# Optimization experiments

Hardware: AMD Instinct MI355X
Metric: run time of the kernel (lower is better)

The kernel has to match this reference:

```python
import jax, jax.numpy as jnp
import numpy as np

NY, NX = 1024, 2048
DX, DT, NU, UB = 1.0, 0.1, 0.01, 1.0
NITER = 5
NLEVEL = int(np.log2(NY)) + 1  # 11
DIAG = -8.0 / (3.0 * DX * DX)  # center coefficient of the Laplacian stencil wA


def _conv(x, w, stride=1):
    # single-channel 'VALID' cross-correlation, same semantics as torch Conv2d(padding=0)
    return jax.lax.conv_general_dilated(x, w, (stride, stride), 'VALID',
                                        dimension_numbers=('NCHW', 'OIHW', 'NCHW'))


def _bc_u(u):
    # inlet (left/top/bottom) = ub, zero-gradient outflow on the right
    uu = jnp.pad(u, ((0, 0), (0, 0), (1, 1), (1, 1)))
    uu = uu.at[:, :, :, 0].set(UB)
    uu = uu.at[:, :, :, -1].set(uu[:, :, :, -2])
    uu = uu.at[:, :, 0, :].set(UB)
    uu = uu.at[:, :, -1, :].set(UB)
    return uu


def _bc_v(v):
    # v = 0 on inlet/top/bottom (zero pad), zero-gradient outflow on the right
    vv = jnp.pad(v, ((0, 0), (0, 0), (1, 1), (1, 1)))
    vv = vv.at[:, :, :, -1].set(vv[:, :, :, -2])
    return vv


def _bc_p(p):
    # zero-gradient pressure except fixed p=0 at the outlet
    pp = jnp.pad(p, ((0, 0), (0, 0), (1, 1), (1, 1)))
    pp = pp.at[:, :, :, 0].set(pp[:, :, :, 1])
    pp = pp.at[:, :, :, -1].set(0.0)
    pp = pp.at[:, :, 0, :].set(pp[:, :, 1, :])
    pp = pp.at[:, :, -1, :].set(pp[:, :, -2, :])
    return pp


def _bc_cw(a):
    # homogeneous (zero) halo for the multigrid correction
    return jnp.pad(a, ((0, 0), (0, 0), (1, 1), (1, 1)))


def _prolong(a):
    return jnp.repeat(jnp.repeat(a, 2, axis=2), 2, axis=3)


def _f_cycle_mg(uu, vv, p, w_xadv, w_yadv, w_A, w_res):
    b = -(_conv(uu, w_xadv) + _conv(vv, w_yadv)) / DT
    for _ in range(NITER):
        r = _conv(_bc_p(p), w_A) - b
        r_s = [r]
        for _i in range(1, NLEVEL):
            r = _conv(r, w_res, stride=2)
            r_s.append(r)
        a = jnp.zeros((1, 1, 1, 1), dtype=p.dtype)
        for i in reversed(range(1, NLEVEL)):
            if i == NLEVEL - 1:
                a = r_s[i] / DIAG
            else:
                a = a - _conv(_bc_cw(a), w_A) / DIAG + r_s[i] / DIAG
            a = _prolong(a)
        p = p - a
        p = p - _conv(_bc_p(p), w_A) / DIAG + b / DIAG
    return p


def _forward(u, v, p, sigma, w_xadv, w_yadv, w_diff, w_A, w_res):
    uu, vv, pp = _bc_u(u), _bc_v(v), _bc_p(p)
    Grapx_p = _conv(pp, w_xadv) * DT
    Grapy_p = _conv(pp, w_yadv) * DT
    ADx_u, ADy_u = _conv(uu, w_xadv), _conv(uu, w_yadv)
    ADx_v, ADy_v = _conv(vv, w_xadv), _conv(vv, w_yadv)
    AD2_u, AD2_v = _conv(uu, w_diff), _conv(vv, w_diff)
    # predictor half-step
    bu = u + 0.5 * (NU * AD2_u * DT - u * ADx_u * DT - v * ADy_u * DT) - Grapx_p
    bv = v + 0.5 * (NU * AD2_v * DT - u * ADx_v * DT - v * ADy_v * DT) - Grapy_p
    damp = 1.0 / (1.0 + DT * sigma)  # solid body Brinkman penalty
    bu, bv = bu * damp, bv * damp
    buu, bvv = _bc_u(bu), _bc_v(bv)
    ADx_u, ADy_u = _conv(buu, w_xadv), _conv(buu, w_yadv)
    ADx_v, ADy_v = _conv(bvv, w_xadv), _conv(bvv, w_yadv)
    AD2_u, AD2_v = _conv(buu, w_diff), _conv(bvv, w_diff)
    # corrector step
    u = u + NU * AD2_u * DT - bu * ADx_u * DT - bv * ADy_u * DT - Grapx_p
    v = v + NU * AD2_v * DT - bu * ADx_v * DT - bv * ADy_v * DT - Grapy_p
    u, v = u * damp, v * damp
    uu, vv = _bc_u(u), _bc_v(v)
    # pressure solve via multigrid F-cycle + projection
    p = _f_cycle_mg(uu, vv, p, w_xadv, w_yadv, w_A, w_res)
    pp = _bc_p(p)
    u = u - _conv(pp, w_xadv) * DT
    v = v - _conv(pp, w_yadv) * DT
    u, v = u * damp, v * damp
    return jnp.concatenate([u, v, p], axis=1)  # (1, 3, NY, NX)


def setup_inputs() -> dict:
    key = jax.random.key(0)
    k1, k2, k3 = jax.random.split(key, 3)
    shp = (1, 1, NY, NX)
    u = jax.random.normal(k1, shp, jnp.float32) * 0.1 + UB
    v = jax.random.normal(k2, shp, jnp.float32) * 0.1
    p = jax.random.normal(k3, shp, jnp.float32) * 0.1
    # bluff-body mask: 1/timescale inside the rectangle (Block.create_solid_body_2D)
    cor_x, cor_y = NX // 4, NY // 2
    size_x, size_y = NX // 32, NY // 8
    sigma = jnp.zeros(shp, jnp.float32)
    sigma = sigma.at[0, 0, cor_y - size_y:cor_y + size_y,
                     cor_x - size_x:cor_x + size_x].set(1e8)
    # finite-difference stencils from get_weights_linear_2D(dx)
    w_diff = jnp.array([[1., 1., 1.], [1., -8., 1.], [1., 1., 1.]],
                       jnp.float32).reshape(1, 1, 3, 3) / (3.0 * DX * DX)
    w_xadv = jnp.array([[-1., 0., 1.], [-4., 0., 4.], [-1., 0., 1.]],
                       jnp.float32).reshape(1, 1, 3, 3) / (12.0 * DX)
    w_yadv = jnp.array([[-1., -4., -1.], [0., 0., 0.], [1., 4., 1.]],
                       jnp.float32).reshape(1, 1, 3, 3) / (12.0 * DX)
    w_A = w_diff
    w_res = jnp.full((1, 1, 2, 2), 0.25, jnp.float32)
    return {"u": u, "v": v, "p": p, "sigma": sigma, "w_xadv": w_xadv,
            "w_yadv": w_yadv, "w_diff": w_diff, "w_A": w_A, "w_res": w_res}


def reference(u, v, p, sigma, w_xadv, w_yadv, w_diff, w_A, w_res):
    return _forward(u, v, p, sigma, w_xadv, w_yadv, w_diff, w_A, w_res)
```

## Files before the change

kernel.cpp:

```cpp
#include <hip/hip_runtime.h>
#include <cstdint>

#define GNY 1024
#define GNX 2048
#define GNPTS (GNY * GNX)

namespace {
constexpr float DT = 0.1f;
constexpr float NUc = 0.01f;
constexpr float INV_DIAG = -0.375f;
}

__device__ __forceinline__ float bc_u_at(const float* __restrict__ f, int y, int x) {
    if (y < 0 || y >= GNY || x < 0) return 1.0f;
    if (x >= GNX) x = GNX - 1;
    return f[y * GNX + x];
}
__device__ __forceinline__ float bc_v_at(const float* __restrict__ f, int y, int x) {
    if (y < 0 || y >= GNY || x < 0) return 0.0f;
    if (x >= GNX) x = GNX - 1;
    return f[y * GNX + x];
}
__device__ __forceinline__ float bc_p_at(const float* __restrict__ f, int y, int x) {
    if (x >= GNX) return 0.0f;
    if (x < 0) x = 0;
    y = min(max(y, 0), GNY - 1);
    return f[y * GNX + x];
}

__device__ __forceinline__ float conv_x3(const float m[3][3]) {
    return ((m[0][2] - m[0][0]) + 4.0f * (m[1][2] - m[1][0]) + (m[2][2] - m[2][0])) * (1.0f / 12.0f);
}
__device__ __forceinline__ float conv_y3(const float m[3][3]) {
    return ((m[2][0] - m[0][0]) + 4.0f * (m[2][1] - m[0][1]) + (m[2][2] - m[0][2])) * (1.0f / 12.0f);
}
__device__ __forceinline__ float conv_d3(const float m[3][3]) {
    return (m[0][0] + m[0][1] + m[0][2] + m[1][0] + m[1][2] + m[2][0] + m[2][1] + m[2][2]
            - 8.0f * m[1][1]) * (1.0f / 3.0f);
}

__device__ __forceinline__ float strip_d3(const float* b0, const float* b1, const float* b2, int k) {
    float cs0 = b0[k] + b1[k] + b2[k];
    float cs1 = b0[k+1] + b1[k+1] + b2[k+1];
    float cs2 = b0[k+2] + b1[k+2] + b2[k+2];
    return (cs0 + cs1 + cs2 - 9.0f * b1[k+1]) * (1.0f / 3.0f);
}
__device__ __forceinline__ float strip_x3(const float* b0, const float* b1, const float* b2, int k) {
    return ((b0[k+2] + 4.0f*b1[k+2] + b2[k+2]) - (b0[k] + 4.0f*b1[k] + b2[k])) * (1.0f / 12.0f);
}
__device__ __forceinline__ float strip_y3(const float* b0, const float* b1, const float* b2, int k) {
    return ((b2[k] - b0[k]) + 4.0f*(b2[k+1] - b0[k+1]) + (b2[k+2] - b0[k+2])) * (1.0f / 12.0f);
}
#define STRIP_LOAD(arr, base, stride) \
    { _Pragma("unroll") for (int j = 0; j < 6; ++j) { \
        b0[j] = arr[(base) + j]; b1[j] = arr[(base) + (stride) + j]; b2[j] = arr[(base) + 2*(stride) + j]; } }

__global__ __launch_bounds__(256) void k_front(
        const float* __restrict__ u, const float* __restrict__ v,
        const float* __restrict__ p, const float* __restrict__ sigma,
        float* __restrict__ u2g, float* __restrict__ v2g, float* __restrict__ bg,
        float* __restrict__ r1, float* __restrict__ r2, float* __restrict__ r3,
        float* __restrict__ r4, float* __restrict__ r5) {
    __shared__ float scrF[7110];
    float* sP    = scrF;
    float* sU    = scrF + 1482;
    float* sV    = scrF + 2964;
    float* sU2   = scrF + 1482;
    float* sV2   = scrF + 2672;
    float* sBu   = scrF + 4446;
    float* sBv   = scrF + 5778;
    float* s0    = scrF + 4446;
    float* s1    = scrF + 5502;
    float* s2    = scrF + 5774;
    float* s3    = scrF + 5846;
    float* s4    = scrF + 5866;

    int t = threadIdx.x;
    int bx = blockIdx.x, by = blockIdx.y;
    int y0 = by * 32, x0 = bx * 32;
    bool edge = !(bx >= 1 && bx <= 62 && by >= 1 && by <= 30);
    bool rightcol = (bx == 63);

    if (!edge) {
        for (int i = t; i < 1444; i += 256) {
            int wy = i / 38, wx = i - wy * 38;
            int idx = (y0 - 3 + wy) * GNX + (x0 - 3 + wx);
            sP[wy * 39 + wx] = p[idx];
            sU[wy * 39 + wx] = u[idx];
            sV[wy * 39 + wx] = v[idx];
        }
    } else {
        for (int i = t; i < 1444; i += 256) {
            int wy = i / 38, wx = i - wy * 38;
            int gy = y0 - 3 + wy, gx = x0 - 3 + wx;
            sP[wy * 39 + wx] = bc_p_at(p, gy, gx);
            sU[wy * 39 + wx] = bc_u_at(u, gy, gx);
            sV[wy * 39 + wx] = bc_v_at(v, gy, gx);
        }
    }
    __syncthreads();

    if (!edge) {
        for (int s = t; s < 324; s += 256) {
            int ay = s / 9, ax0 = (s - (s / 9) * 9) * 4;
            int base = ay * 39 + ax0;
            float b0[6], b1[6], b2[6];
            float d3u[4], x3u[4], y3u[4], uc4[4];
            STRIP_LOAD(sU, base, 39)
#pragma unroll
            for (int k = 0; k < 4; ++k) {
                uc4[k] = b1[k+1];
                d3u[k] = strip_d3(b0, b1, b2, k);
                x3u[k] = strip_x3(b0, b1, b2, k);
                y3u[k] = strip_y3(b0, b1, b2, k);
            }
            float d3v[4], x3v[4], y3v[4], vc4[4];
            STRIP_LOAD(sV, base, 39)
#pragma unroll
            for (int k = 0; k < 4; ++k) {
                vc4[k] = b1[k+1];
                d3v[k] = strip_d3(b0, b1, b2, k);
                x3v[k] = strip_x3(b0, b1, b2, k);
                y3v[k] = strip_y3(b0, b1, b2, k);
            }
            float gx4[4], gy4[4];
            STRIP_LOAD(sP, base, 39)
#pragma unroll
            for (int k = 0; k < 4; ++k) {
                gx4[k] = strip_x3(b0, b1, b2, k) * DT;
                gy4[k] = strip_y3(b0, b1, b2, k) * DT;
            }
#pragma unroll
            for (int k = 0; k < 4; ++k) {
                int gy = y0 - 2 + ay, gx = x0 - 2 + ax0 + k;
                float dampv = 1.0f / (1.0f + DT * sigma[gy * GNX + gx]);
                float buv = (uc4[k] + 0.5f * (NUc * d3u[k] * DT - uc4[k] * x3u[k] * DT - vc4[k] * y3u[k] * DT) - gx4[k]) * dampv;
                float bvv = (vc4[k] + 0.5f * (NUc * d3v[k] * DT - uc4[k] * x3v[k] * DT - vc4[k] * y3v[k] * DT) - gy4[k]) * dampv;
                sBu[ay * 37 + ax0 + k] = buv;
                sBv[ay * 37 + ax0 + k] = bvv;
            }
        }
    } else {
        for (int i = t; i < 1296; i += 256) {
            int ay = i / 36, ax = i - ay * 36;
            int gy = y0 - 2 + ay, gx = x0 - 2 + ax;
            float un[3][3], vn[3][3], pn[3][3];
#pragma unroll
            for (int dy = 0; dy < 3; ++dy)
#pragma unroll
                for (int dx = 0; dx < 3; ++dx) {
                    int li = (ay + dy) * 39 + ax + dx;
                    un[dy][dx] = sU[li]; vn[dy][dx] = sV[li]; pn[dy][dx] = sP[li];
                }
            float buv, bvv;
            bool valid = (gy >= 0 && gy < GNY && gx >= 0 && gx < GNX);
            if (valid) {
                float dampv = 1.0f / (1.0f + DT * sigma[gy * GNX + gx]);
                float gxp = conv_x3(pn) * DT, gyp = conv_y3(pn) * DT;
                float uc = un[1][1], vc = vn[1][1];
                buv = (uc + 0.5f * (NUc * conv_d3(un) * DT - uc * conv_x3(un) * DT - vc * conv_y3(un) * DT) - gxp) * dampv;
                bvv = (vc + 0.5f * (NUc * conv_d3(vn) * DT - uc * conv_x3(vn) * DT - vc * conv_y3(vn) * DT) - gyp) * dampv;
            } else if (gy < 0 || gy >= GNY || gx < 0) {
                buv = 1.0f; bvv = 0.0f;
            } else {
                buv = 0.0f; bvv = 0.0f;
            }
            sBu[ay * 37 + ax] = buv;
            sBv[ay * 37 + ax] = bvv;
        }
    }
    __syncthreads();

    float ucS[2][4], vcS[2][4];
    float ucA[5], vcA[5];
    if (!edge) {
        int ns = 0;
        for (int s = t; s < 306; s += 256, ++ns) {
            int cy = s / 9, cx0 = (s - (s / 9) * 9) * 4;
#pragma unroll
            for (int k = 0; k < 4; ++k) {
                if (cx0 + k < 34) {
                    int li = (cy + 2) * 39 + cx0 + 2 + k;
                    ucS[ns][k] = sU[li]; vcS[ns][k] = sV[li];
                }
            }
        }
    } else {
        int np = 0;
        for (int i = t; i < 1156; i += 256, ++np) {
            int cy = i / 34, cx = i - cy * 34;
            int li = (cy + 2) * 39 + cx + 2;
            ucA[np] = sU[li]; vcA[np] = sV[li];
        }
    }
    __syncthreads();
    if (!edge) {
        int ns = 0;
        for (int s = t; s < 306; s += 256, ++ns) {
            int cy = s / 9, cx0 = (s - (s / 9) * 9) * 4;
            int baseB = cy * 37 + cx0;
            int baseP = (cy + 1) * 39 + cx0 + 1;
            float b0[6], b1[6], b2[6];
            float d3bu[4], x3bu[4], y3bu[4], buc4[4];
            STRIP_LOAD(sBu, baseB, 37)
#pragma unroll
            for (int k = 0; k < 4; ++k) {
                buc4[k] = b1[k+1];
                d3bu[k] = strip_d3(b0, b1, b2, k);
                x3bu[k] = strip_x3(b0, b1, b2, k);
                y3bu[k] = strip_y3(b0, b1, b2, k);
            }
            float d3bv[4], x3bv[4], y3bv[4], bvc4[4];
            STRIP_LOAD(sBv, baseB, 37)
#pragma unroll
            for (int k = 0; k < 4; ++k) {
                bvc4[k] = b1[k+1];
                d3bv[k] = strip_d3(b0, b1, b2, k);
                x3bv[k] = strip_x3(b0, b1, b2, k);
                y3bv[k] = strip_y3(b0, b1, b2, k);
            }
            float gx4[4], gy4[4];
            STRIP_LOAD(sP, baseP, 39)
#pragma unroll
            for (int k = 0; k < 4; ++k) {
                gx4[k] = strip_x3(b0, b1, b2, k) * DT;
                gy4[k] = strip_y3(b0, b1, b2, k) * DT;
            }
#pragma unroll
            for (int k = 0; k < 4; ++k) {
                if (cx0 + k < 34) {
                    int cy_ = cy, cx_ = cx0 + k;
                    int gyy = y0 - 1 + cy_, gxx = x0 - 1 + cx_;
                    int idx = gyy * GNX + gxx;
                    float dampv = 1.0f / (1.0f + DT * sigma[idx]);
                    float u2_ = (ucS[ns][k] + NUc * d3bu[k] * DT - buc4[k] * x3bu[k] * DT - bvc4[k] * y3bu[k] * DT - gx4[k]) * dampv;
                    float v2_ = (vcS[ns][k] + NUc * d3bv[k] * DT - buc4[k] * x3bv[k] * DT - bvc4[k] * y3bv[k] * DT - gy4[k]) * dampv;
                    if (cy_ >= 1 && cy_ <= 32 && cx_ >= 1 && cx_ <= 32) {
                        u2g[idx] = u2_; v2g[idx] = v2_;
                    }
                    sU2[cy_ * 35 + cx_] = u2_;
                    sV2[cy_ * 35 + cx_] = v2_;
                }
            }
        }
    } else {
        int np = 0;
        for (int i = t; i < 1156; i += 256, ++np) {
            int cy = i / 34, cx = i - cy * 34;
            int gy = y0 - 1 + cy, gx = x0 - 1 + cx;
            float u2_ = 0.0f, v2_ = 0.0f;
            bool valid = (gy >= 0 && gy < GNY && gx >= 0 && gx < GNX);
            if (valid) {
                float bun[3][3], bvn[3][3], pn[3][3];
                if (!rightcol) {
#pragma unroll
                    for (int dy = 0; dy < 3; ++dy)
#pragma unroll
                        for (int dx = 0; dx < 3; ++dx) {
                            int li = (cy + dy) * 37 + cx + dx;
                            bun[dy][dx] = sBu[li]; bvn[dy][dx] = sBv[li];
                            pn[dy][dx] = sP[(cy + dy + 1) * 39 + cx + dx + 1];
                        }
                } else {
#pragma unroll
                    for (int dy = 0; dy < 3; ++dy)
#pragma unroll
                        for (int dx = 0; dx < 3; ++dx) {
                            int yy = gy + dy - 1, xx = gx + dx - 1;
                            pn[dy][dx] = sP[(cy + dy + 1) * 39 + cx + dx + 1];
                            if (yy < 0 || yy >= GNY || xx < 0) { bun[dy][dx] = 1.0f; bvn[dy][dx] = 0.0f; }
                            else {
                                int cxx = (xx >= GNX) ? GNX - 1 : xx;
                                int li = (cy + dy) * 37 + (cxx - (x0 - 2));
                                bun[dy][dx] = sBu[li]; bvn[dy][dx] = sBv[li];
                            }
                        }
                }
                int idx = gy * GNX + gx;
                float gxp = conv_x3(pn) * DT, gyp = conv_y3(pn) * DT;
                float dampv = 1.0f / (1.0f + DT * sigma[idx]);
                float buc = bun[1][1], bvc = bvn[1][1];
                u2_ = (ucA[np] + NUc * conv_d3(bun) * DT - buc * conv_x3(bun) * DT - bvc * conv_y3(bun) * DT - gxp) * dampv;
                v2_ = (vcA[np] + NUc * conv_d3(bvn) * DT - buc * conv_x3(bvn) * DT - bvc * conv_y3(bvn) * DT - gyp) * dampv;
                if (cy >= 1 && cy <= 32 && cx >= 1 && cx <= 32) {
                    u2g[idx] = u2_; v2g[idx] = v2_;
                }
            } else if (gy < 0 || gy >= GNY || gx < 0) {
                u2_ = 1.0f; v2_ = 0.0f;
            }
            sU2[cy * 35 + cx] = u2_;
            sV2[cy * 35 + cx] = v2_;
        }
    }
    __syncthreads();

    if (!rightcol) {
        int ty = t >> 3, tx0 = (t & 7) * 4;
        int baseU = ty * 35 + tx0;
        int baseP = (ty + 2) * 39 + tx0 + 2;
        float b0[6], b1[6], b2[6];
        float x3u[4];
        STRIP_LOAD(sU2, baseU, 35)
#pragma unroll
        for (int k = 0; k < 4; ++k) x3u[k] = strip_x3(b0, b1, b2, k);
        float y3v[4];
        STRIP_LOAD(sV2, baseU, 35)
#pragma unroll
        for (int k = 0; k < 4; ++k) y3v[k] = strip_y3(b0, b1, b2, k);
        float d3p[4];
        STRIP_LOAD(sP, baseP, 39)
#pragma unroll
        for (int k = 0; k < 4; ++k) d3p[k] = strip_d3(b0, b1, b2, k);
#pragma unroll
        for (int k = 0; k < 4; ++k) {
            float b_ = -(x3u[k] + y3v[k]) * (1.0f / DT);
            bg[(y0 + ty) * GNX + x0 + tx0 + k] = b_;
            s0[ty * 33 + tx0 + k] = d3p[k] - b_;
        }
    } else {
        for (int i = t; i < 1024; i += 256) {
            int ty = i >> 5, tx = i & 31;
            int gy = y0 + ty, gx = x0 + tx;
            float un[3][3], vn[3][3], pn[3][3];
#pragma unroll
            for (int dy = 0; dy < 3; ++dy)
#pragma unroll
                for (int dx = 0; dx < 3; ++dx) {
                    int yy = gy + dy - 1, xx = gx + dx - 1;
                    pn[dy][dx] = sP[(ty + dy + 2) * 39 + tx + dx + 2];
                    if (yy < 0 || yy >= GNY || xx < 0) { un[dy][dx] = 1.0f; vn[dy][dx] = 0.0f; }
                    else {
                        int cxx = (xx >= GNX) ? GNX - 1 : xx;
                        int li = (ty + dy) * 35 + (cxx - (x0 - 1));
                        un[dy][dx] = sU2[li]; vn[dy][dx] = sV2[li];
                    }
                }
            float b_ = -(conv_x3(un) + conv_y3(vn)) * (1.0f / DT);
            bg[gy * GNX + gx] = b_;
            s0[ty * 33 + tx] = conv_d3(pn) - b_;
        }
    }
    __syncthreads();

    { int qy = t >> 4, qx = t & 15;
      float vv = 0.25f * (s0[(2*qy)*33 + 2*qx] + s0[(2*qy)*33 + 2*qx + 1]
                        + s0[(2*qy+1)*33 + 2*qx] + s0[(2*qy+1)*33 + 2*qx + 1]);
      s1[qy*17 + qx] = vv;
      r1[(by*16 + qy)*1024 + bx*16 + qx] = vv; }
    __syncthreads();
    if (t < 64) { int qy = t >> 3, qx = t & 7;
      float vv = 0.25f * (s1[(2*qy)*17 + 2*qx] + s1[(2*qy)*17 + 2*qx + 1]
                        + s1[(2*qy+1)*17 + 2*qx] + s1[(2*qy+1)*17 + 2*qx + 1]);
      s2[qy*9 + qx] = vv;
      r2[(by*8 + qy)*512 + bx*8 + qx] = vv; }
    __syncthreads();
    if (t < 16) { int qy = t >> 2, qx = t & 3;
      float vv = 0.25f * (s2[(2*qy)*9 + 2*qx] + s2[(2*qy)*9 + 2*qx + 1]
                        + s2[(2*qy+1)*9 + 2*qx] + s2[(2*qy+1)*9 + 2*qx + 1]);
      s3[qy*5 + qx] = vv;
      r3[(by*4 + qy)*256 + bx*4 + qx] = vv; }
    __syncthreads();
    if (t < 4) { int qy = t >> 1, qx = t & 1;
      float vv = 0.25f * (s3[(2*qy)*5 + 2*qx] + s3[(2*qy)*5 + 2*qx + 1]
                        + s3[(2*qy+1)*5 + 2*qx] + s3[(2*qy+1)*5 + 2*qx + 1]);
      s4[qy*3 + qx] = vv;
      r4[(by*2 + qy)*128 + bx*2 + qx] = vv; }
    __syncthreads();
    if (t == 0)
        r5[by*64 + bx] = 0.25f * (s4[0] + s4[1] + s4[3] + s4[4]);
}

__global__ __launch_bounds__(256) void k_mg(
        const float* __restrict__ p_src, const float* __restrict__ b,
        const float* __restrict__ r1, const float* __restrict__ r2,
        const float* __restrict__ r3, const float* __restrict__ r4,
        const float* __restrict__ r5,
        float* __restrict__ p_dst,
        float* __restrict__ o1, float* __restrict__ o2, float* __restrict__ o3,
        float* __restrict__ o4, float* __restrict__ o5,
        const float* __restrict__ sigma, float* __restrict__ u_io,
        float* __restrict__ v_io, int last) {
    __shared__ float scr[3948];
    __shared__ float w6v[9], w5v[9], w4v[16], w3v[36], w2v[100], w1v[324];
    float* s5  = scr;
    float* s6  = scr + 2048;
    float* s7  = scr + 2560;
    float* s8  = scr + 2688;
    float* s9  = scr + 2720;
    float* s10 = scr + 2728;
    float* a9  = scr + 2730;
    float* a8  = scr + 2738;
    float* a7  = scr + 2770;
    float* sPp = scr;
    float* sPn = scr + 1332;
    float* s0  = scr + 2522;
    float* s1  = scr + 3578;
    float* s2  = scr + 3850;
    float* s3  = scr + 3922;
    float* s4  = scr + 3942;

    int t = threadIdx.x;
    int bx = blockIdx.x, by = blockIdx.y;
    int y0 = by * 32, x0 = bx * 32;
    bool interior = (bx >= 1 && bx <= 62 && by >= 1 && by <= 30);

    for (int i = t; i < 2048; i += 256) s5[i] = r5[i];
    __syncthreads();
    for (int i = t; i < 512; i += 256) {
        int y = i >> 5, x = i & 31;
        s6[i] = 0.25f * (s5[(2*y)*64 + 2*x] + s5[(2*y)*64 + 2*x + 1]
                       + s5[(2*y+1)*64 + 2*x] + s5[(2*y+1)*64 + 2*x + 1]);
    }
    __syncthreads();
    if (t < 128) { int y = t >> 4, x = t & 15;
        s7[t] = 0.25f * (s6[(2*y)*32 + 2*x] + s6[(2*y)*32 + 2*x + 1]
                       + s6[(2*y+1)*32 + 2*x] + s6[(2*y+1)*32 + 2*x + 1]); }
    __syncthreads();
    if (t < 32) { int y = t >> 3, x = t & 7;
        s8[t] = 0.25f * (s7[(2*y)*16 + 2*x] + s7[(2*y)*16 + 2*x + 1]
                       + s7[(2*y+1)*16 + 2*x] + s7[(2*y+1)*16 + 2*x + 1]); }
    __syncthreads();
    if (t < 8) { int y = t >> 2, x = t & 3;
        s9[t] = 0.25f * (s8[(2*y)*8 + 2*x] + s8[(2*y)*8 + 2*x + 1]
                       + s8[(2*y+1)*8 + 2*x] + s8[(2*y+1)*8 + 2*x + 1]); }
    __syncthreads();
    if (t < 2)
        s10[t] = 0.25f * (s9[2*t] + s9[2*t + 1] + s9[4 + 2*t] + s9[4 + 2*t + 1]);
    __syncthreads();

    auto upv = [&](auto pget, float rval, int H, int W, int y, int x) -> float {
        float m[3][3];
#pragma unroll
        for (int dy = 0; dy < 3; ++dy)
#pragma unroll
            for (int dx = 0; dx < 3; ++dx) {
                int yy = y + dy - 1, xx = x + dx - 1;
                m[dy][dx] = (yy >= 0 && yy < H && xx >= 0 && xx < W) ? pget(yy >> 1, xx >> 1) : 0.0f;
            }
        float conv = (m[0][0] + m[0][1] + m[0][2] + m[1][0] + m[1][2]
                      + m[2][0] + m[2][1] + m[2][2] - 8.0f * m[1][1]) * (1.0f / 3.0f);
        return m[1][1] - conv * INV_DIAG + rval * INV_DIAG;
    };

    if (t < 8) { int y = t >> 2, x = t & 3;
        a9[t] = upv([&](int py, int px) { return s10[py*2 + px] * INV_DIAG; },
                    s9[t], 2, 4, y, x); }
    __syncthreads();
    if (t < 32) { int y = t >> 3, x = t & 7;
        a8[t] = upv([&](int py, int px) { return a9[py*4 + px]; },
                    s8[t], 4, 8, y, x); }
    __syncthreads();
    if (t < 128) { int y = t >> 4, x = t & 15;
        a7[t] = upv([&](int py, int px) { return a8[py*8 + px]; },
                    s7[t], 8, 16, y, x); }
    __syncthreads();

    int w6ylo = (by - 2) >> 1, w6xlo = (bx - 2) >> 1;
    int w5ylo = by - 1,        w5xlo = bx - 1;
    int w4ylo = 2*by - 1,      w4xlo = 2*bx - 1;
    int w3ylo = 4*by - 1,      w3xlo = 4*bx - 1;
    int w2ylo = 8*by - 1,      w2xlo = 8*bx - 1;
    int w1ylo = 16*by - 1,     w1xlo = 16*bx - 1;

    if (t < 9) { int gy = w6ylo + t/3, gx = w6xlo + t%3;
        w6v[t] = (gy >= 0 && gy < 16 && gx >= 0 && gx < 32)
            ? upv([&](int py, int px) { return a7[py*16 + px]; },
                  s6[gy*32 + gx], 16, 32, gy, gx) : 0.0f; }
    __syncthreads();
    if (t < 9) { int gy = w5ylo + t/3, gx = w5xlo + t%3;
        w5v[t] = (gy >= 0 && gy < 32 && gx >= 0 && gx < 64)
            ? upv([&](int py, int px) { return w6v[(py - w6ylo)*3 + (px - w6xlo)]; },
                  s5[gy*64 + gx], 32, 64, gy, gx) : 0.0f; }
    __syncthreads();
    if (t < 16) { int gy = w4ylo + t/4, gx = w4xlo + t%4;
        w4v[t] = (gy >= 0 && gy < 64 && gx >= 0 && gx < 128)
            ? upv([&](int py, int px) { return w5v[(py - w5ylo)*3 + (px - w5xlo)]; },
                  r4[gy*128 + gx], 64, 128, gy, gx) : 0.0f; }
    __syncthreads();
    if (t < 36) { int gy = w3ylo + t/6, gx = w3xlo + t%6;
        w3v[t] = (gy >= 0 && gy < 128 && gx >= 0 && gx < 256)
            ? upv([&](int py, int px) { return w4v[(py - w4ylo)*4 + (px - w4xlo)]; },
                  r3[gy*256 + gx], 128, 256, gy, gx) : 0.0f; }
    __syncthreads();
    if (t < 100) { int gy = w2ylo + t/10, gx = w2xlo + t%10;
        w2v[t] = (gy >= 0 && gy < 256 && gx >= 0 && gx < 512)
            ? upv([&](int py, int px) { return w3v[(py - w3ylo)*6 + (px - w3xlo)]; },
                  r2[gy*512 + gx], 256, 512, gy, gx) : 0.0f; }
    __syncthreads();
    for (int i = t; i < 324; i += 256) { int gy = w1ylo + i/18, gx = w1xlo + i%18;
        w1v[i] = (gy >= 0 && gy < 512 && gx >= 0 && gx < 1024)
            ? upv([&](int py, int px) { return w2v[(py - w2ylo)*10 + (px - w2xlo)]; },
                  r1[gy*1024 + gx], 512, 1024, gy, gx) : 0.0f; }
    __syncthreads();

    for (int i = t; i < 1296; i += 256) {
        int wy = i / 36, wx = i - wy * 36;
        int yy = y0 - 2 + wy, xx = x0 - 2 + wx;
        float v = 0.0f;
        if (xx < GNX) {
            int cy = min(max(yy, 0), GNY - 1);
            int cx = xx < 0 ? 0 : xx;
            v = p_src[cy*GNX + cx] - w1v[((cy >> 1) - w1ylo)*18 + ((cx >> 1) - w1xlo)];
        }
        sPp[wy*37 + wx] = v;
    }
    __syncthreads();
    if (interior) {
        for (int s = t; s < 306; s += 256) {
            int wy = s / 9, wx0 = (s - (s / 9) * 9) * 4;
            int base = wy * 37 + wx0;
            float b0[6], b1[6], b2[6];
            STRIP_LOAD(sPp, base, 37)
#pragma unroll
            for (int k = 0; k < 4; ++k) {
                if (wx0 + k < 34) {
                    float c = b1[k+1];
                    float conv = strip_d3(b0, b1, b2, k);
                    float bvv = b[(y0 - 1 + wy) * GNX + (x0 - 1 + wx0 + k)];
                    sPn[wy * 35 + wx0 + k] = c - conv * INV_DIAG + bvv * INV_DIAG;
                }
            }
        }
    } else {
        for (int i = t; i < 1156; i += 256) {
            int wy = i / 34, wx = i - wy * 34;
            int yy = y0 - 1 + wy, xx = x0 - 1 + wx;
            float v = 0.0f;
            if (xx < GNX) {
                int cy = min(max(yy, 0), GNY - 1);
                int cx = xx < 0 ? 0 : xx;
                int rb = cy - y0 + 2, cb = cx - x0 + 2;
                float m[3][3];
#pragma unroll
                for (int dy = 0; dy < 3; ++dy)
#pragma unroll
                    for (int dx = 0; dx < 3; ++dx)
                        m[dy][dx] = sPp[(rb + dy - 1)*37 + (cb + dx - 1)];
                float conv = (m[0][0] + m[0][1] + m[0][2] + m[1][0] + m[1][2]
                              + m[2][0] + m[2][1] + m[2][2] - 8.0f*m[1][1]) * (1.0f / 3.0f);
                v = m[1][1] - conv * INV_DIAG + b[cy*GNX + cx] * INV_DIAG;
            }
            sPn[wy*35 + wx] = v;
        }
    }
    __syncthreads();
    for (int i = t; i < 1024; i += 256) {
        int ty = i >> 5, tx = i & 31;
        p_dst[(y0 + ty)*GNX + x0 + tx] = sPn[(ty + 1)*35 + (tx + 1)];
    }

    if (!last) {
        {
            int ty = t >> 3, tx0 = (t & 7) * 4;
            int base = ty * 35 + tx0;
            float b0[6], b1[6], b2[6];
            STRIP_LOAD(sPn, base, 35)
#pragma unroll
            for (int k = 0; k < 4; ++k) {
                float d3 = strip_d3(b0, b1, b2, k);
                s0[ty * 33 + tx0 + k] = d3 - b[(y0 + ty) * GNX + x0 + tx0 + k];
            }
        }
        __syncthreads();
        { int qy = t >> 4, qx = t & 15;
          float v = 0.25f * (s0[(2*qy)*33 + 2*qx] + s0[(2*qy)*33 + 2*qx + 1]
                           + s0[(2*qy+1)*33 + 2*qx] + s0[(2*qy+1)*33 + 2*qx + 1]);
          s1[qy*17 + qx] = v;
          o1[(by*16 + qy)*1024 + bx*16 + qx] = v; }
        __syncthreads();
        if (t < 64) { int qy = t >> 3, qx = t & 7;
          float v = 0.25f * (s1[(2*qy)*17 + 2*qx] + s1[(2*qy)*17 + 2*qx + 1]
                           + s1[(2*qy+1)*17 + 2*qx] + s1[(2*qy+1)*17 + 2*qx + 1]);
          s2[qy*9 + qx] = v;
          o2[(by*8 + qy)*512 + bx*8 + qx] = v; }
        __syncthreads();
        if (t < 16) { int qy = t >> 2, qx = t & 3;
          float v = 0.25f * (s2[(2*qy)*9 + 2*qx] + s2[(2*qy)*9 + 2*qx + 1]
                           + s2[(2*qy+1)*9 + 2*qx] + s2[(2*qy+1)*9 + 2*qx + 1]);
          s3[qy*5 + qx] = v;
          o3[(by*4 + qy)*256 + bx*4 + qx] = v; }
        __syncthreads();
        if (t < 4) { int qy = t >> 1, qx = t & 1;
          float v = 0.25f * (s3[(2*qy)*5 + 2*qx] + s3[(2*qy)*5 + 2*qx + 1]
                           + s3[(2*qy+1)*5 + 2*qx] + s3[(2*qy+1)*5 + 2*qx + 1]);
          s4[qy*3 + qx] = v;
          o4[(by*2 + qy)*128 + bx*2 + qx] = v; }
        __syncthreads();
        if (t == 0)
            o5[by*64 + bx] = 0.25f * (s4[0] + s4[1] + s4[3] + s4[4]);
    } else {
        int ty = t >> 3, tx0 = (t & 7) * 4;
        int base = ty * 35 + tx0;
        float b0[6], b1[6], b2[6];
        float x3p[4], y3p[4];
        STRIP_LOAD(sPn, base, 35)
#pragma unroll
        for (int k = 0; k < 4; ++k) {
            x3p[k] = strip_x3(b0, b1, b2, k);
            y3p[k] = strip_y3(b0, b1, b2, k);
        }
#pragma unroll
        for (int k = 0; k < 4; ++k) {
            int idx = (y0 + ty) * GNX + x0 + tx0 + k;
            float damp = 1.0f / (1.0f + DT * sigma[idx]);
            u_io[idx] = (u_io[idx] - x3p[k] * DT) * damp;
            v_io[idx] = (v_io[idx] - y3p[k] * DT) * damp;
        }
    }
}

extern "C" void kernel_launch(void* const* d_in, const int* in_sizes, int n_in,
                              void* d_out, int out_size, void* d_ws, size_t ws_size,
                              hipStream_t stream) {
    (void)in_sizes; (void)n_in; (void)out_size; (void)ws_size;
    const float* u_in  = (const float*)d_in[0];
    const float* v_in  = (const float*)d_in[1];
    const float* p_in  = (const float*)d_in[2];
    const float* sigma = (const float*)d_in[3];

    float* out_u = (float*)d_out;
    float* out_v = out_u + GNPTS;
    float* out_p = out_u + 2 * (size_t)GNPTS;

    float* ws   = (float*)d_ws;
    float* b    = ws;
    float* p_ws = b + (size_t)GNPTS;
    float* base = p_ws + (size_t)GNPTS;
    float* A_[5], * B_[5];
    size_t lsz[5] = {524288, 131072, 32768, 8192, 2048};
    float* cur = base;
    for (int l = 0; l < 5; ++l) { A_[l] = cur; cur += lsz[l]; }
    for (int l = 0; l < 5; ++l) { B_[l] = cur; cur += lsz[l]; }

    dim3 grdT(GNX / 32, GNY / 32), blkT(256);

    k_front<<<grdT, blkT, 0, stream>>>(u_in, v_in, p_in, sigma,
                                       out_u, out_v, b,
                                       A_[0], A_[1], A_[2], A_[3], A_[4]);

    const float* p_cur = p_in;
    float* p_bufs[2] = { out_p, p_ws };
    for (int it = 0; it < 5; ++it) {
        float** rp = (it % 2 == 0) ? A_ : B_;
        float** wp = (it % 2 == 0) ? B_ : A_;
        float* p_next = p_bufs[it % 2];
        int last = (it == 4) ? 1 : 0;
        k_mg<<<grdT, blkT, 0, stream>>>(p_cur, b,
                                        rp[0], rp[1], rp[2], rp[3], rp[4],
                                        p_next,
                                        wp[0], wp[1], wp[2], wp[3], wp[4],
                                        sigma, out_u, out_v, last);
        p_cur = p_next;
    }
}
```

Baseline: 219.9 us.

## Use 6-wide stencil strips and swizzle block indices for locality

Interior stencil passes now give each thread 6 output columns instead of 4. This removes the second loop trip for threads past 256, so each pass fits in one wave of work with fewer redundant shared-memory halo reads per output. Block IDs are remapped with a swizzle so that consecutively scheduled blocks cover nearby tiles, which is meant to improve L2 locality for halo reuse. Shared arrays are padded slightly to absorb the wider strip reads. The cost is higher register pressure and some threads idling in the last group.

```diff
diff --git a/kernel.cpp b/kernel.cpp
--- a/kernel.cpp
+++ b/kernel.cpp
@@ -9,6 +9,13 @@
 constexpr float DT = 0.1f;
 constexpr float NUc = 0.01f;
 constexpr float INV_DIAG = -0.375f;
+}
+
+__device__ __forceinline__ void swizzle_bid(int& bx, int& by) {
+    int n = blockIdx.y * 64 + blockIdx.x;
+    int i = n >> 3;
+    bx = i & 63;
+    by = ((n & 7) << 2) | (i >> 6);
 }
 
 __device__ __forceinline__ float bc_u_at(const float* __restrict__ f, int y, int x) {
@@ -53,6 +60,9 @@
 }
 #define STRIP_LOAD(arr, base, stride) \
     { _Pragma("unroll") for (int j = 0; j < 6; ++j) { \
+        b0[j] = arr[(base) + j]; b1[j] = arr[(base) + (stride) + j]; b2[j] = arr[(base) + 2*(stride) + j]; } }
+#define STRIP6_LOAD(arr, base, stride) \
+    { _Pragma("unroll") for (int j = 0; j < 8; ++j) { \
         b0[j] = arr[(base) + j]; b1[j] = arr[(base) + (stride) + j]; b2[j] = arr[(base) + 2*(stride) + j]; } }
 
 __global__ __launch_bounds__(256) void k_front(
@@ -61,7 +71,7 @@
         float* __restrict__ u2g, float* __restrict__ v2g, float* __restrict__ bg,
         float* __restrict__ r1, float* __restrict__ r2, float* __restrict__ r3,
         float* __restrict__ r4, float* __restrict__ r5) {
-    __shared__ float scrF[7110];
+    __shared__ float scrF[7120];
     float* sP    = scrF;
     float* sU    = scrF + 1482;
     float* sV    = scrF + 2964;
@@ -76,7 +86,8 @@
     float* s4    = scrF + 5866;
 
     int t = threadIdx.x;
-    int bx = blockIdx.x, by = blockIdx.y;
+    int bx, by;
+    swizzle_bid(bx, by);
     int y0 = by * 32, x0 = bx * 32;
     bool edge = !(bx >= 1 && bx <= 62 && by >= 1 && by <= 30);
     bool rightcol = (bx == 63);
@@ -101,41 +112,41 @@
     __syncthreads();
 
     if (!edge) {
-        for (int s = t; s < 324; s += 256) {
-            int ay = s / 9, ax0 = (s - (s / 9) * 9) * 4;
+        if (t < 216) {
+            int ay = t / 6, ax0 = (t - (t / 6) * 6) * 6;
             int base = ay * 39 + ax0;
-            float b0[6], b1[6], b2[6];
-            float d3u[4], x3u[4], y3u[4], uc4[4];
-            STRIP_LOAD(sU, base, 39)
-#pragma unroll
-            for (int k = 0; k < 4; ++k) {
-                uc4[k] = b1[k+1];
+            float b0[8], b1[8], b2[8];
+            float d3u[6], x3u[6], y3u[6], uc6[6];
+            STRIP6_LOAD(sU, base, 39)
+#pragma unroll
+            for (int k = 0; k < 6; ++k) {
+                uc6[k] = b1[k+1];
                 d3u[k] = strip_d3(b0, b1, b2, k);
                 x3u[k] = strip_x3(b0, b1, b2, k);
                 y3u[k] = strip_y3(b0, b1, b2, k);
             }
-            float d3v[4], x3v[4], y3v[4], vc4[4];
-            STRIP_LOAD(sV, base, 39)
-#pragma unroll
-            for (int k = 0; k < 4; ++k) {
-                vc4[k] = b1[k+1];
+            float d3v[6], x3v[6], y3v[6], vc6[6];
+            STRIP6_LOAD(sV, base, 39)
+#pragma unroll
+            for (int k = 0; k < 6; ++k) {
+                vc6[k] = b1[k+1];
                 d3v[k] = strip_d3(b0, b1, b2, k);
                 x3v[k] = strip_x3(b0, b1, b2, k);
                 y3v[k] = strip_y3(b0, b1, b2, k);
             }
-            float gx4[4], gy4[4];
-            STRIP_LOAD(sP, base, 39)
-#pragma unroll
-            for (int k = 0; k < 4; ++k) {
-                gx4[k] = strip_x3(b0, b1, b2, k) * DT;
-                gy4[k] = strip_y3(b0, b1, b2, k) * DT;
-            }
-#pragma unroll
-            for (int k = 0; k < 4; ++k) {
+            float gx6[6], gy6[6];
+            STRIP6_LOAD(sP, base, 39)
+#pragma unroll
+            for (int k = 0; k < 6; ++k) {
+                gx6[k] = strip_x3(b0, b1, b2, k) * DT;
+                gy6[k] = strip_y3(b0, b1, b2, k) * DT;
+            }
+#pragma unroll
+            for (int k = 0; k < 6; ++k) {
                 int gy = y0 - 2 + ay, gx = x0 - 2 + ax0 + k;
                 float dampv = 1.0f / (1.0f + DT * sigma[gy * GNX + gx]);
-                float buv = (uc4[k] + 0.5f * (NUc * d3u[k] * DT - uc4[k] * x3u[k] * DT - vc4[k] * y3u[k] * DT) - gx4[k]) * dampv;
-                float bvv = (vc4[k] + 0.5f * (NUc * d3v[k] * DT - uc4[k] * x3v[k] * DT - vc4[k] * y3v[k] * DT) - gy4[k]) * dampv;
+                float buv = (uc6[k] + 0.5f * (NUc * d3u[k] * DT - uc6[k] * x3u[k] * DT - vc6[k] * y3u[k] * DT) - gx6[k]) * dampv;
+                float bvv = (vc6[k] + 0.5f * (NUc * d3v[k] * DT - uc6[k] * x3v[k] * DT - vc6[k] * y3v[k] * DT) - gy6[k]) * dampv;
                 sBu[ay * 37 + ax0 + k] = buv;
                 sBv[ay * 37 + ax0 + k] = bvv;
             }
@@ -171,17 +182,16 @@
     }
     __syncthreads();
 
-    float ucS[2][4], vcS[2][4];
+    float ucS[6], vcS[6];
     float ucA[5], vcA[5];
     if (!edge) {
-        int ns = 0;
-        for (int s = t; s < 306; s += 256, ++ns) {
-            int cy = s / 9, cx0 = (s - (s / 9) * 9) * 4;
-#pragma unroll
-            for (int k = 0; k < 4; ++k) {
+        if (t < 204) {
+            int cy = t / 6, cx0 = (t - (t / 6) * 6) * 6;
+#pragma unroll
+            for (int k = 0; k < 6; ++k) {
                 if (cx0 + k < 34) {
                     int li = (cy + 2) * 39 + cx0 + 2 + k;
-                    ucS[ns][k] = sU[li]; vcS[ns][k] = sV[li];
+                    ucS[k] = sU[li]; vcS[k] = sV[li];
                 }
             }
         }
@@ -195,51 +205,50 @@
     }
     __syncthreads();
     if (!edge) {
-        int ns = 0;
-        for (int s = t; s < 306; s += 256, ++ns) {
-            int cy = s / 9, cx0 = (s - (s / 9) * 9) * 4;
+        if (t < 204) {
+            int cy = t / 6, cx0 = (t - (t / 6) * 6) * 6;
             int baseB = cy * 37 + cx0;
             int baseP = (cy + 1) * 39 + cx0 + 1;
-            float b0[6], b1[6], b2[6];
-            float d3bu[4], x3bu[4], y3bu[4], buc4[4];
-            STRIP_LOAD(sBu, baseB, 37)
-#pragma unroll
-            for (int k = 0; k < 4; ++k) {
-                buc4[k] = b1[k+1];
+            float b0[8], b1[8], b2[8];
+            float d3bu[6], x3bu[6], y3bu[6], buc6[6];
+            STRIP6_LOAD(sBu, baseB, 37)
+#pragma unroll
+            for (int k = 0; k < 6; ++k) {
+                buc6[k] = b1[k+1];
                 d3bu[k] = strip_d3(b0, b1, b2, k);
                 x3bu[k] = strip_x3(b0, b1, b2, k);
                 y3bu[k] = strip_y3(b0, b1, b2, k);
             }
-            float d3bv[4], x3bv[4], y3bv[4], bvc4[4];
-            STRIP_LOAD(sBv, baseB, 37)
-#pragma unroll
-            for (int k = 0; k < 4; ++k) {
-                bvc4[k] = b1[k+1];
+            float d3bv[6], x3bv[6], y3bv[6], bvc6[6];
+            STRIP6_LOAD(sBv, baseB, 37)
+#pragma unroll
+            for (int k = 0; k < 6; ++k) {
+                bvc6[k] = b1[k+1];
                 d3bv[k] = strip_d3(b0, b1, b2, k);
                 x3bv[k] = strip_x3(b0, b1, b2, k);
                 y3bv[k] = strip_y3(b0, b1, b2, k);
             }
-            float gx4[4], gy4[4];
-            STRIP_LOAD(sP, baseP, 39)
-#pragma unroll
-            for (int k = 0; k < 4; ++k) {
-                gx4[k] = strip_x3(b0, b1, b2, k) * DT;
-                gy4[k] = strip_y3(b0, b1, b2, k) * DT;
-            }
-#pragma unroll
-            for (int k = 0; k < 4; ++k) {
+            float gx6[6], gy6[6];
+            STRIP6_LOAD(sP, baseP, 39)
+#pragma unroll
+            for (int k = 0; k < 6; ++k) {
+                gx6[k] = strip_x3(b0, b1, b2, k) * DT;
+                gy6[k] = strip_y3(b0, b1, b2, k) * DT;
+            }
+#pragma unroll
+            for (int k = 0; k < 6; ++k) {
                 if (cx0 + k < 34) {
-                    int cy_ = cy, cx_ = cx0 + k;
-                    int gyy = y0 - 1 + cy_, gxx = x0 - 1 + cx_;
+                    int cx_ = cx0 + k;
+                    int gyy = y0 - 1 + cy, gxx = x0 - 1 + cx_;
                     int idx = gyy * GNX + gxx;
                     float dampv = 1.0f / (1.0f + DT * sigma[idx]);
-                    float u2_ = (ucS[ns][k] + NUc * d3bu[k] * DT - buc4[k] * x3bu[k] * DT - bvc4[k] * y3bu[k] * DT - gx4[k]) * dampv;
-                    float v2_ = (vcS[ns][k] + NUc * d3bv[k] * DT - buc4[k] * x3bv[k] * DT - bvc4[k] * y3bv[k] * DT - gy4[k]) * dampv;
-                    if (cy_ >= 1 && cy_ <= 32 && cx_ >= 1 && cx_ <= 32) {
+                    float u2_ = (ucS[k] + NUc * d3bu[k] * DT - buc6[k] * x3bu[k] * DT - bvc6[k] * y3bu[k] * DT - gx6[k]) * dampv;
+                    float v2_ = (vcS[k] + NUc * d3bv[k] * DT - buc6[k] * x3bv[k] * DT - bvc6[k] * y3bv[k] * DT - gy6[k]) * dampv;
+                    if (cy >= 1 && cy <= 32 && cx_ >= 1 && cx_ <= 32) {
                         u2g[idx] = u2_; v2g[idx] = v2_;
                     }
-                    sU2[cy_ * 35 + cx_] = u2_;
-                    sV2[cy_ * 35 + cx_] = v2_;
+                    sU2[cy * 35 + cx_] = u2_;
+                    sV2[cy * 35 + cx_] = v2_;
                 }
             }
         }
@@ -380,7 +389,7 @@
         float* __restrict__ o4, float* __restrict__ o5,
         const float* __restrict__ sigma, float* __restrict__ u_io,
         float* __restrict__ v_io, int last) {
-    __shared__ float scr[3948];
+    __shared__ float scr[3958];
     __shared__ float w6v[9], w5v[9], w4v[16], w3v[36], w2v[100], w1v[324];
     float* s5  = scr;
     float* s6  = scr + 2048;
@@ -400,7 +409,8 @@
     float* s4  = scr + 3942;
 
     int t = threadIdx.x;
-    int bx = blockIdx.x, by = blockIdx.y;
+    int bx, by;
+    swizzle_bid(bx, by);
     int y0 = by * 32, x0 = bx * 32;
     bool interior = (bx >= 1 && bx <= 62 && by >= 1 && by <= 30);
 
@@ -506,13 +516,13 @@
     }
     __syncthreads();
     if (interior) {
-        for (int s = t; s < 306; s += 256) {
-            int wy = s / 9, wx0 = (s - (s / 9) * 9) * 4;
+        if (t < 204) {
+            int wy = t / 6, wx0 = (t - (t / 6) * 6) * 6;
             int base = wy * 37 + wx0;
-            float b0[6], b1[6], b2[6];
-            STRIP_LOAD(sPp, base, 37)
-#pragma unroll
-            for (int k = 0; k < 4; ++k) {
+            float b0[8], b1[8], b2[8];
+            STRIP6_LOAD(sPp, base, 37)
+#pragma unroll
+            for (int k = 0; k < 6; ++k) {
                 if (wx0 + k < 34) {
                     float c = b1[k+1];
                     float conv = strip_d3(b0, b1, b2, k);
```

Result: faster. 195.0 us (-11.3%).
